# Performance work log

Hardware: AMD Instinct MI355X
Metric: run time of the kernel (lower is better)

The kernel has to match this reference:

```python
import jax, jax.numpy as jnp
import numpy as np

N = 1_000_000
C = 32
DIMS = (480, 360, 32)  # cylindrical voxel grid (z/rho, phi, height)
EPS = 1e-5


def setup_inputs() -> dict:
    rng = np.random.default_rng(0)
    total = DIMS[0] * DIMS[1] * DIMS[2]
    # unique active voxels, sorted so searchsorted gives row indices directly
    ids = np.sort(rng.choice(total, size=N, replace=False)).astype(np.int64)
    z = ids // (DIMS[1] * DIMS[2])
    rem = ids % (DIMS[1] * DIMS[2])
    y = rem // DIMS[2]
    x = rem % DIMS[2]
    coords = np.stack([z, y, x], axis=1)
    strides = np.array([DIMS[1] * DIMS[2], DIMS[2], 1], dtype=np.int64)

    def nbr(delta):
        out = np.full((3, N), -1, dtype=np.int32)
        for a in range(3):
            tgt = ids + delta * strides[a]
            ok = (coords[:, a] + delta >= 0) & (coords[:, a] + delta < DIMS[a])
            pos = np.searchsorted(ids, tgt)
            pos_c = np.clip(pos, 0, N - 1)
            found = ok & (ids[pos_c] == tgt)
            out[a] = np.where(found, pos_c, -1).astype(np.int32)
        return out

    nbr_prev = nbr(-1)
    nbr_next = nbr(+1)

    key = jax.random.key(0)
    k0, k1, k2 = jax.random.split(key, 3)
    features = jax.random.normal(k0, (N, C), dtype=jnp.float32)
    # W[branch, tap, in, out]; taps ordered (-1, 0, +1) along the branch's axis
    W = jax.random.normal(k1, (3, 3, C, C), dtype=jnp.float32) * (1.0 / np.sqrt(3 * C))
    gamma = jnp.ones((3, C), dtype=jnp.float32)
    beta = jnp.zeros((3, C), dtype=jnp.float32)
    mean = jax.random.normal(k2, (3, C), dtype=jnp.float32) * 0.1
    var = jnp.ones((3, C), dtype=jnp.float32)
    return {
        "features": features,
        "nbr_prev": jnp.asarray(nbr_prev),
        "nbr_next": jnp.asarray(nbr_next),
        "W": W,
        "gamma": gamma,
        "beta": beta,
        "mean": mean,
        "var": var,
    }


def _branch(f, Wb, prev, nxt, g, b, m, v):
    # 3-tap submanifold conv along one axis: gather prev/next active neighbors
    pm = prev >= 0
    nm = nxt >= 0
    fp = jnp.where(pm[:, None], f[jnp.where(pm, prev, 0)], 0.0)
    fn = jnp.where(nm[:, None], f[jnp.where(nm, nxt, 0)], 0.0)
    out = fp @ Wb[0] + f @ Wb[1] + fn @ Wb[2]
    # BatchNorm1d (inference stats) + Sigmoid
    out = (out - m) * (g * jax.lax.rsqrt(v + EPS)) + b
    return jax.nn.sigmoid(out)


def reference(features, nbr_prev, nbr_next, W, gamma, beta, mean, var):
    acc = jnp.zeros_like(features)
    for a in range(3):  # conv3x1x1, conv1x3x1, conv1x1x3
        acc = acc + _branch(features, W[a], nbr_prev[a], nbr_next[a],
                            gamma[a], beta[a], mean[a], var[a])
    return acc * features  # sparse_add then gating with input features
```

## Files before the change

kernel.cpp:

```cpp
#include <hip/hip_runtime.h>
#include <stdint.h>


typedef __attribute__((ext_vector_type(8))) __bf16 bf16x8;
typedef __attribute__((ext_vector_type(8))) unsigned short u16x8;
typedef __attribute__((ext_vector_type(4))) float f32x4;
typedef __attribute__((ext_vector_type(2))) float f32x2;

constexpr int NVOX    = 1000000;
constexpr int NTILES  = NVOX / 16;
constexpr int WPB     = 4;
constexpr float LOG2E = 1.4426950408889634f;

constexpr int TPW4     = 4;
constexpr int NWAVES4  = NTILES / TPW4;
constexpr int NBLOCKS4 = (NWAVES4 + WPB - 1) / WPB;

constexpr int TPW2     = 2;
constexpr int NWAVES2  = (NTILES + TPW2 - 1) / TPW2;
constexpr int NBLOCKS2 = (NWAVES2 + WPB - 1) / WPB;

constexpr int    WS_WELEMS = 18 * 64 * 8;
constexpr size_t FB_BYTES  = (size_t)NVOX * 64;
constexpr unsigned ZOFF    = (unsigned)(FB_BYTES + 18432 + 768);
constexpr size_t WS_NEED   = FB_BYTES + 18432 + 768 + 128;

__global__ __launch_bounds__(256) void prep_kernel(
    const float* __restrict__ Wt,
    const float* __restrict__ gma, const float* __restrict__ bta,
    const float* __restrict__ mea, const float* __restrict__ var,
    unsigned short* __restrict__ wsW, float* __restrict__ wsA,
    float* __restrict__ wsB, float* __restrict__ wsZ)
{
    int tid = blockIdx.x * 256 + threadIdx.x;
    if (tid < WS_WELEMS) {
        int f    = tid >> 9;
        int rem  = tid & 511;
        int lane = rem >> 3;
        int j    = rem & 7;
        int br = f / 6, t = (f >> 1) % 3, h = f & 1;
        int n = lane & 15, quad = lane >> 4;
        float w = Wt[((br * 3 + t) * 32 + quad * 8 + j) * 32 + 2 * n + h];
        union { float f; unsigned u; } c; c.f = w;
        wsW[(f * 64 + lane) * 8 + j] = (unsigned short)((c.u + 0x8000u) >> 16);
    } else if (tid < WS_WELEMS + 96) {
        int i = tid - WS_WELEMS;
        float s = gma[i] * __frsqrt_rn(var[i] + 1e-5f);
        wsA[i] = -s * LOG2E;
        wsB[i] = (mea[i] * s - bta[i]) * LOG2E;
    } else if (wsZ != nullptr && tid < WS_WELEMS + 96 + 32) {
        wsZ[tid - WS_WELEMS - 96] = 0.0f;
    }
}

__device__ __forceinline__ unsigned pack_bf(float a, float b) {
    union { float f; unsigned u; } ca, cb; ca.f = a; cb.f = b;
    return __builtin_amdgcn_perm(cb.u + 0x8000u, ca.u + 0x8000u, 0x07060302u);
}
__device__ __forceinline__ bf16x8 cvt_frag(f32x4 lo, f32x4 hi) {
    union { unsigned u[4]; bf16x8 v; } r;
    r.u[0] = pack_bf(lo[0], lo[1]); r.u[1] = pack_bf(lo[2], lo[3]);
    r.u[2] = pack_bf(hi[0], hi[1]); r.u[3] = pack_bf(hi[2], hi[3]);
    return r.v;
}

__global__ __launch_bounds__(256) void cvt_feat(
    const float* __restrict__ f, unsigned short* __restrict__ fb)
{
    int tid = blockIdx.x * 256 + threadIdx.x;
    const f32x4* p = (const f32x4*)(f + (size_t)tid * 8);
    f32x4 lo = p[0], hi = p[1];
    union { unsigned u[4]; u16x8 v; } r;
    r.u[0] = pack_bf(lo[0], lo[1]); r.u[1] = pack_bf(lo[2], lo[3]);
    r.u[2] = pack_bf(hi[0], hi[1]); r.u[3] = pack_bf(hi[2], hi[3]);
    *(u16x8*)(fb + (size_t)tid * 8) = r.v;
}

__device__ __forceinline__ f32x4 mfma16(u16x8 a, bf16x8 b, f32x4 c) {
    return __builtin_amdgcn_mfma_f32_16x16x32_bf16(
        __builtin_bit_cast(bf16x8, a), b, c, 0, 0, 0);
}

__global__ __launch_bounds__(256) void recon_bf16(
    const float* __restrict__ feat,
    const int*   __restrict__ nprev,
    const int*   __restrict__ nnext,
    const char*  __restrict__ fbc,
    const unsigned short* __restrict__ wsW,
    const float* __restrict__ wsA,
    const float* __restrict__ wsB,
    float*       __restrict__ out)
{
    __shared__ unsigned short smem[WS_WELEMS];
    {
        const u16x8* s = (const u16x8*)wsW;
        u16x8* d = (u16x8*)smem;
        #pragma unroll
        for (int i = 0; i < 5; ++i) {
            int k = (int)threadIdx.x + i * 256;
            if (k < 18 * 64) d[k] = s[k];
        }
    }
    __syncthreads();

    const int lane = threadIdx.x & 63;
    const int n    = lane & 15;
    const int quad = lane >> 4;
    const unsigned qo = (unsigned)quad * 16u;

    int b   = blockIdx.x;
    int per = NBLOCKS4 / 8;
    int bs  = (b < per * 8) ? ((b & 7) * per + (b >> 3)) : b;
    int wv  = bs * WPB + (threadIdx.x >> 6);
    if (wv >= NWAVES4) return;
    const int t0 = wv * TPW4;

    f32x2 A_[3], B_[3];
    #pragma unroll
    for (int br = 0; br < 3; ++br) {
        A_[br] = *(const f32x2*)(wsA + br * 32 + 2 * n);
        B_[br] = *(const f32x2*)(wsB + br * 32 + 2 * n);
    }

    unsigned lbase = (unsigned)lane * 16u;

    int idxP[2][3], idxN[2][3];
    {
        int r0 = t0 * 16 + n;
        #pragma unroll
        for (int a = 0; a < 3; ++a) {
            idxP[0][a] = nprev[a * NVOX + r0];
            idxN[0][a] = nnext[a * NVOX + r0];
            idxP[1][a] = nprev[a * NVOX + r0 + 16];
            idxN[1][a] = nnext[a * NVOX + r0 + 16];
        }
    }

    u16x8 G[2][7];
    {
        int row0 = t0 * 16 + n;
        G[0][0] = *(const u16x8*)(fbc + (unsigned)row0 * 64u + qo);
        #pragma unroll
        for (int a = 0; a < 3; ++a) {
            unsigned op = idxP[0][a] >= 0 ? (unsigned)idxP[0][a] * 64u : ZOFF;
            unsigned on = idxN[0][a] >= 0 ? (unsigned)idxN[0][a] * 64u : ZOFF;
            G[0][1 + a] = *(const u16x8*)(fbc + op + qo);
            G[0][4 + a] = *(const u16x8*)(fbc + on + qo);
        }
    }

    #pragma unroll
    for (int tt = 0; tt < TPW4; ++tt) {
        const int cur  = tt & 1;
        const int nxt  = cur ^ 1;
        const int base = (t0 + tt) * 16;

        f32x2 fv[4];
        #pragma unroll
        for (int r = 0; r < 4; ++r)
            fv[r] = __builtin_nontemporal_load(
                (const f32x2*)(feat + (base + quad * 4 + r) * 32 + 2 * n));

        if (tt + 1 < TPW4) {
            int rown = base + 16 + n;
            G[nxt][0] = *(const u16x8*)(fbc + (unsigned)rown * 64u + qo);
            #pragma unroll
            for (int a = 0; a < 3; ++a) {
                unsigned op = idxP[nxt][a] >= 0 ? (unsigned)idxP[nxt][a] * 64u : ZOFF;
                unsigned on = idxN[nxt][a] >= 0 ? (unsigned)idxN[nxt][a] * 64u : ZOFF;
                G[nxt][1 + a] = *(const u16x8*)(fbc + op + qo);
                G[nxt][4 + a] = *(const u16x8*)(fbc + on + qo);
            }
        }
        if (tt + 2 < TPW4) {
            int r2 = base + 32 + n;
            #pragma unroll
            for (int a = 0; a < 3; ++a) {
                idxP[cur][a] = nprev[a * NVOX + r2];
                idxN[cur][a] = nnext[a * NVOX + r2];
            }
        }

        asm volatile("" : "+v"(lbase));
        const char* sb = (const char*)smem + lbase;

        f32x4 acc0 = {0.f, 0.f, 0.f, 0.f}, acc1 = {0.f, 0.f, 0.f, 0.f};
        #pragma unroll
        for (int br = 0; br < 3; ++br) {
            bf16x8 w0 = *(const bf16x8*)(sb + (br * 6 + 0) * 1024);
            bf16x8 w1 = *(const bf16x8*)(sb + (br * 6 + 1) * 1024);
            bf16x8 w2 = *(const bf16x8*)(sb + (br * 6 + 2) * 1024);
            bf16x8 w3 = *(const bf16x8*)(sb + (br * 6 + 3) * 1024);
            bf16x8 w4 = *(const bf16x8*)(sb + (br * 6 + 4) * 1024);
            bf16x8 w5 = *(const bf16x8*)(sb + (br * 6 + 5) * 1024);
            f32x4 c0 = {0.f, 0.f, 0.f, 0.f}, c1 = {0.f, 0.f, 0.f, 0.f};
            c0 = mfma16(G[cur][1 + br], w0, c0);
            c1 = mfma16(G[cur][1 + br], w1, c1);
            c0 = mfma16(G[cur][0],      w2, c0);
            c1 = mfma16(G[cur][0],      w3, c1);
            c0 = mfma16(G[cur][4 + br], w4, c0);
            c1 = mfma16(G[cur][4 + br], w5, c1);
            float a0 = A_[br][0], b0 = B_[br][0];
            float a1 = A_[br][1], b1 = B_[br][1];
            #pragma unroll
            for (int r = 0; r < 4; ++r) {
                float e0 = __builtin_amdgcn_exp2f(__builtin_fmaf(c0[r], a0, b0));
                float e1 = __builtin_amdgcn_exp2f(__builtin_fmaf(c1[r], a1, b1));
                acc0[r] += __builtin_amdgcn_rcpf(1.0f + e0);
                acc1[r] += __builtin_amdgcn_rcpf(1.0f + e1);
            }
        }

        #pragma unroll
        for (int r = 0; r < 4; ++r) {
            int vrow = base + quad * 4 + r;
            f32x2 ov = { acc0[r] * fv[r][0], acc1[r] * fv[r][1] };
            __builtin_nontemporal_store(ov, (f32x2*)(out + vrow * 32 + 2 * n));
        }
    }
}

__global__ __launch_bounds__(256) void recon_legacy(
    const float*          __restrict__ feat,
    const int*            __restrict__ nprev,
    const int*            __restrict__ nnext,
    const unsigned short* __restrict__ wsW,
    const float*          __restrict__ wsA,
    const float*          __restrict__ wsB,
    float*                __restrict__ out)
{
    const int lane = threadIdx.x & 63;
    const int n    = lane & 15;
    const int quad = lane >> 4;

    int b   = blockIdx.x;
    int per = NBLOCKS2 / 8;
    int bs  = (b < per * 8) ? ((b & 7) * per + (b >> 3)) : b;
    int wv  = bs * WPB + (threadIdx.x >> 6);

    const int t0 = wv * TPW2;
    if (t0 >= NTILES) return;

    bf16x8 Bf[18];
    #pragma unroll
    for (int f = 0; f < 18; ++f)
        Bf[f] = __builtin_bit_cast(bf16x8, *(const u16x8*)(wsW + (f * 64 + lane) * 8));

    f32x2 A_[3], B_[3];
    #pragma unroll
    for (int br = 0; br < 3; ++br) {
        A_[br] = *(const f32x2*)(wsA + br * 32 + 2 * n);
        B_[br] = *(const f32x2*)(wsB + br * 32 + 2 * n);
    }

    int ip[3], inx[3];
    {
        int row0 = t0 * 16 + n;
        #pragma unroll
        for (int a = 0; a < 3; ++a) {
            ip[a]  = nprev[a * NVOX + row0];
            inx[a] = nnext[a * NVOX + row0];
        }
    }

    #pragma unroll 1
    for (int tt = 0; tt < TPW2; ++tt) {
        int tile = t0 + tt;
        if (tile >= NTILES) break;
        int base = tile * 16;
        int row  = base + n;

        const f32x4* ps = (const f32x4*)(feat + row * 32 + quad * 8);
        f32x4 s_lo = ps[0], s_hi = ps[1];
        f32x4 p_lo[3], p_hi[3], n_lo[3], n_hi[3];
        #pragma unroll
        for (int a = 0; a < 3; ++a) {
            p_lo[a] = (f32x4){0.f, 0.f, 0.f, 0.f}; p_hi[a] = p_lo[a];
            n_lo[a] = p_lo[a];                     n_hi[a] = p_lo[a];
            if (ip[a] >= 0) {
                const f32x4* pp = (const f32x4*)(feat + ip[a] * 32 + quad * 8);
                p_lo[a] = pp[0]; p_hi[a] = pp[1];
            }
            if (inx[a] >= 0) {
                const f32x4* pn = (const f32x4*)(feat + inx[a] * 32 + quad * 8);
                n_lo[a] = pn[0]; n_hi[a] = pn[1];
            }
        }

        int ipn[3], inn[3];
        if (tt + 1 < TPW2 && tile + 1 < NTILES) {
            int nrow = row + 16;
            #pragma unroll
            for (int a = 0; a < 3; ++a) {
                ipn[a] = nprev[a * NVOX + nrow];
                inn[a] = nnext[a * NVOX + nrow];
            }
        } else {
            #pragma unroll
            for (int a = 0; a < 3; ++a) { ipn[a] = -1; inn[a] = -1; }
        }

        bf16x8 Aself = cvt_frag(s_lo, s_hi);
        bf16x8 Ap[3], An[3];
        #pragma unroll
        for (int a = 0; a < 3; ++a) {
            Ap[a] = cvt_frag(p_lo[a], p_hi[a]);
            An[a] = cvt_frag(n_lo[a], n_hi[a]);
        }

        f32x4 acc0 = {0.f, 0.f, 0.f, 0.f}, acc1 = {0.f, 0.f, 0.f, 0.f};
        #pragma unroll
        for (int br = 0; br < 3; ++br) {
            f32x4 c0 = {0.f, 0.f, 0.f, 0.f}, c1 = {0.f, 0.f, 0.f, 0.f};
            c0 = __builtin_amdgcn_mfma_f32_16x16x32_bf16(Ap[br], Bf[br*6 + 0], c0, 0, 0, 0);
            c1 = __builtin_amdgcn_mfma_f32_16x16x32_bf16(Ap[br], Bf[br*6 + 1], c1, 0, 0, 0);
            c0 = __builtin_amdgcn_mfma_f32_16x16x32_bf16(Aself,  Bf[br*6 + 2], c0, 0, 0, 0);
            c1 = __builtin_amdgcn_mfma_f32_16x16x32_bf16(Aself,  Bf[br*6 + 3], c1, 0, 0, 0);
            c0 = __builtin_amdgcn_mfma_f32_16x16x32_bf16(An[br], Bf[br*6 + 4], c0, 0, 0, 0);
            c1 = __builtin_amdgcn_mfma_f32_16x16x32_bf16(An[br], Bf[br*6 + 5], c1, 0, 0, 0);
            float a0 = A_[br][0], b0 = B_[br][0], a1 = A_[br][1], b1 = B_[br][1];
            #pragma unroll
            for (int r = 0; r < 4; ++r) {
                float e0 = __builtin_amdgcn_exp2f(__builtin_fmaf(c0[r], a0, b0));
                float e1 = __builtin_amdgcn_exp2f(__builtin_fmaf(c1[r], a1, b1));
                acc0[r] += __builtin_amdgcn_rcpf(1.0f + e0);
                acc1[r] += __builtin_amdgcn_rcpf(1.0f + e1);
            }
        }

        #pragma unroll
        for (int r = 0; r < 4; ++r) {
            int vrow = base + quad * 4 + r;
            f32x2 fv = *(const f32x2*)(feat + vrow * 32 + 2 * n);
            f32x2 ov = { acc0[r] * fv[0], acc1[r] * fv[1] };
            *(f32x2*)(out + vrow * 32 + 2 * n) = ov;
        }

        #pragma unroll
        for (int a = 0; a < 3; ++a) { ip[a] = ipn[a]; inx[a] = inn[a]; }
    }
}

extern "C" void kernel_launch(void* const* d_in, const int* in_sizes, int n_in,
                              void* d_out, int out_size, void* d_ws, size_t ws_size,
                              hipStream_t stream) {
    const float* feat  = (const float*)d_in[0];
    const int*   nprev = (const int*)d_in[1];
    const int*   nnext = (const int*)d_in[2];
    const float* Wt    = (const float*)d_in[3];
    const float* gma   = (const float*)d_in[4];
    const float* bta   = (const float*)d_in[5];
    const float* mea   = (const float*)d_in[6];
    const float* var   = (const float*)d_in[7];
    float*       o     = (float*)d_out;

    if (ws_size >= WS_NEED) {
        unsigned short* fb  = (unsigned short*)d_ws;
        unsigned short* wsW = (unsigned short*)((char*)d_ws + FB_BYTES);
        float* wsA = (float*)((char*)d_ws + FB_BYTES + 18432);
        float* wsB = wsA + 96;
        float* wsZ = wsB + 96;
        prep_kernel<<<(WS_WELEMS + 96 + 32 + 255) / 256, 256, 0, stream>>>(
            Wt, gma, bta, mea, var, wsW, wsA, wsB, wsZ);
        cvt_feat<<<(NVOX * 32) / (256 * 8), 256, 0, stream>>>(feat, fb);
        recon_bf16<<<NBLOCKS4, 256, 0, stream>>>(feat, nprev, nnext,
            (const char*)d_ws, wsW, wsA, wsB, o);
    } else {
        unsigned short* wsW = (unsigned short*)d_ws;
        float* wsA = (float*)((char*)d_ws + WS_WELEMS * 2);
        float* wsB = wsA + 96;
        prep_kernel<<<(WS_WELEMS + 96 + 255) / 256, 256, 0, stream>>>(
            Wt, gma, bta, mea, var, wsW, wsA, wsB, nullptr);
        recon_legacy<<<NBLOCKS2, 256, 0, stream>>>(feat, nprev, nnext,
                                                   wsW, wsA, wsB, o);
    }
}
```

Before: 304.8 us.

## Fuse weight prep with feature bf16 conversion and raise tiles per wave

Result: no change. 305.9 us (+0.4%).

```diff
diff --git a/kernel.cpp b/kernel.cpp
--- a/kernel.cpp
+++ b/kernel.cpp
@@ -12,9 +12,9 @@
 constexpr int WPB     = 4;
 constexpr float LOG2E = 1.4426950408889634f;
 
-constexpr int TPW4     = 4;
-constexpr int NWAVES4  = NTILES / TPW4;
-constexpr int NBLOCKS4 = (NWAVES4 + WPB - 1) / WPB;
+constexpr int TPWF     = 5;
+constexpr int NWAVESF  = NTILES / TPWF;
+constexpr int NBLOCKSF = NWAVESF / WPB;
 
 constexpr int TPW2     = 2;
 constexpr int NWAVES2  = (NTILES + TPW2 - 1) / TPW2;
@@ -25,7 +25,44 @@
 constexpr unsigned ZOFF    = (unsigned)(FB_BYTES + 18432 + 768);
 constexpr size_t WS_NEED   = FB_BYTES + 18432 + 768 + 128;
 
-__global__ __launch_bounds__(256) void prep_kernel(
+constexpr int CVT_THREADS = NVOX * 32 / 16;
+constexpr int PREP_TAIL   = WS_WELEMS + 96 + 32;
+constexpr int PREPALL_BLK = (CVT_THREADS + PREP_TAIL + 255) / 256;
+
+__device__ __forceinline__ unsigned pack_bf(float a, float b) {
+    union { float f; unsigned u; } ca, cb; ca.f = a; cb.f = b;
+    return __builtin_amdgcn_perm(cb.u + 0x8000u, ca.u + 0x8000u, 0x07060302u);
+}
+
+__device__ __forceinline__ void prep_tail_work(
+    int t, const float* __restrict__ Wt,
+    const float* __restrict__ gma, const float* __restrict__ bta,
+    const float* __restrict__ mea, const float* __restrict__ var,
+    unsigned short* __restrict__ wsW, float* __restrict__ wsA,
+    float* __restrict__ wsB, float* __restrict__ wsZ)
+{
+    if (t < WS_WELEMS) {
+        int f    = t >> 9;
+        int rem  = t & 511;
+        int lane = rem >> 3;
+        int j    = rem & 7;
+        int br = f / 6, tap = (f >> 1) % 3, h = f & 1;
+        int n = lane & 15, quad = lane >> 4;
+        float w = Wt[((br * 3 + tap) * 32 + quad * 8 + j) * 32 + 2 * n + h];
+        union { float f; unsigned u; } c; c.f = w;
+        wsW[(f * 64 + lane) * 8 + j] = (unsigned short)((c.u + 0x8000u) >> 16);
+    } else if (t < WS_WELEMS + 96) {
+        int i = t - WS_WELEMS;
+        float s = gma[i] * __frsqrt_rn(var[i] + 1e-5f);
+        wsA[i] = -s * LOG2E;
+        wsB[i] = (mea[i] * s - bta[i]) * LOG2E;
+    } else if (wsZ != nullptr && t < WS_WELEMS + 96 + 32) {
+        wsZ[t - WS_WELEMS - 96] = 0.0f;
+    }
+}
+
+__global__ __launch_bounds__(256) void prep_all(
+    const float* __restrict__ feat, unsigned short* __restrict__ fb,
     const float* __restrict__ Wt,
     const float* __restrict__ gma, const float* __restrict__ bta,
     const float* __restrict__ mea, const float* __restrict__ var,
@@ -33,47 +70,38 @@
     float* __restrict__ wsB, float* __restrict__ wsZ)
 {
     int tid = blockIdx.x * 256 + threadIdx.x;
-    if (tid < WS_WELEMS) {
-        int f    = tid >> 9;
-        int rem  = tid & 511;
-        int lane = rem >> 3;
-        int j    = rem & 7;
-        int br = f / 6, t = (f >> 1) % 3, h = f & 1;
-        int n = lane & 15, quad = lane >> 4;
-        float w = Wt[((br * 3 + t) * 32 + quad * 8 + j) * 32 + 2 * n + h];
-        union { float f; unsigned u; } c; c.f = w;
-        wsW[(f * 64 + lane) * 8 + j] = (unsigned short)((c.u + 0x8000u) >> 16);
-    } else if (tid < WS_WELEMS + 96) {
-        int i = tid - WS_WELEMS;
-        float s = gma[i] * __frsqrt_rn(var[i] + 1e-5f);
-        wsA[i] = -s * LOG2E;
-        wsB[i] = (mea[i] * s - bta[i]) * LOG2E;
-    } else if (wsZ != nullptr && tid < WS_WELEMS + 96 + 32) {
-        wsZ[tid - WS_WELEMS - 96] = 0.0f;
-    }
-}
-
-__device__ __forceinline__ unsigned pack_bf(float a, float b) {
-    union { float f; unsigned u; } ca, cb; ca.f = a; cb.f = b;
-    return __builtin_amdgcn_perm(cb.u + 0x8000u, ca.u + 0x8000u, 0x07060302u);
-}
+    if (tid < CVT_THREADS) {
+        const f32x4* p = (const f32x4*)(feat + (size_t)tid * 16);
+        f32x4 v0 = p[0], v1 = p[1], v2 = p[2], v3 = p[3];
+        union { unsigned u[8]; u16x8 v[2]; } r;
+        r.u[0] = pack_bf(v0[0], v0[1]); r.u[1] = pack_bf(v0[2], v0[3]);
+        r.u[2] = pack_bf(v1[0], v1[1]); r.u[3] = pack_bf(v1[2], v1[3]);
+        r.u[4] = pack_bf(v2[0], v2[1]); r.u[5] = pack_bf(v2[2], v2[3]);
+        r.u[6] = pack_bf(v3[0], v3[1]); r.u[7] = pack_bf(v3[2], v3[3]);
+        u16x8* q = (u16x8*)(fb + (size_t)tid * 16);
+        q[0] = r.v[0]; q[1] = r.v[1];
+    } else {
+        prep_tail_work(tid - CVT_THREADS, Wt, gma, bta, mea, var,
+                       wsW, wsA, wsB, wsZ);
+    }
+}
+
+__global__ __launch_bounds__(256) void prep_kernel(
+    const float* __restrict__ Wt,
+    const float* __restrict__ gma, const float* __restrict__ bta,
+    const float* __restrict__ mea, const float* __restrict__ var,
+    unsigned short* __restrict__ wsW, float* __restrict__ wsA,
+    float* __restrict__ wsB)
+{
+    int tid = blockIdx.x * 256 + threadIdx.x;
+    prep_tail_work(tid, Wt, gma, bta, mea, var, wsW, wsA, wsB, nullptr);
+}
+
 __device__ __forceinline__ bf16x8 cvt_frag(f32x4 lo, f32x4 hi) {
     union { unsigned u[4]; bf16x8 v; } r;
     r.u[0] = pack_bf(lo[0], lo[1]); r.u[1] = pack_bf(lo[2], lo[3]);
     r.u[2] = pack_bf(hi[0], hi[1]); r.u[3] = pack_bf(hi[2], hi[3]);
     return r.v;
-}
-
-__global__ __launch_bounds__(256) void cvt_feat(
-    const float* __restrict__ f, unsigned short* __restrict__ fb)
-{
-    int tid = blockIdx.x * 256 + threadIdx.x;
-    const f32x4* p = (const f32x4*)(f + (size_t)tid * 8);
-    f32x4 lo = p[0], hi = p[1];
-    union { unsigned u[4]; u16x8 v; } r;
-    r.u[0] = pack_bf(lo[0], lo[1]); r.u[1] = pack_bf(lo[2], lo[3]);
-    r.u[2] = pack_bf(hi[0], hi[1]); r.u[3] = pack_bf(hi[2], hi[3]);
-    *(u16x8*)(fb + (size_t)tid * 8) = r.v;
 }
 
 __device__ __forceinline__ f32x4 mfma16(u16x8 a, bf16x8 b, f32x4 c) {
@@ -109,11 +137,11 @@
     const unsigned qo = (unsigned)quad * 16u;
 
     int b   = blockIdx.x;
-    int per = NBLOCKS4 / 8;
+    int per = NBLOCKSF / 8;
     int bs  = (b < per * 8) ? ((b & 7) * per + (b >> 3)) : b;
     int wv  = bs * WPB + (threadIdx.x >> 6);
-    if (wv >= NWAVES4) return;
-    const int t0 = wv * TPW4;
+    if (wv >= NWAVESF) return;
+    const int t0 = wv * TPWF;
 
     f32x2 A_[3], B_[3];
     #pragma unroll
@@ -129,10 +157,10 @@
         int r0 = t0 * 16 + n;
         #pragma unroll
         for (int a = 0; a < 3; ++a) {
-            idxP[0][a] = nprev[a * NVOX + r0];
-            idxN[0][a] = nnext[a * NVOX + r0];
-            idxP[1][a] = nprev[a * NVOX + r0 + 16];
-            idxN[1][a] = nnext[a * NVOX + r0 + 16];
+            idxP[0][a] = __builtin_nontemporal_load(nprev + a * NVOX + r0);
+            idxN[0][a] = __builtin_nontemporal_load(nnext + a * NVOX + r0);
+            idxP[1][a] = __builtin_nontemporal_load(nprev + a * NVOX + r0 + 16);
+            idxN[1][a] = __builtin_nontemporal_load(nnext + a * NVOX + r0 + 16);
         }
     }
 
@@ -150,7 +178,7 @@
     }
 
     #pragma unroll
-    for (int tt = 0; tt < TPW4; ++tt) {
+    for (int tt = 0; tt < TPWF; ++tt) {
         const int cur  = tt & 1;
         const int nxt  = cur ^ 1;
         const int base = (t0 + tt) * 16;
@@ -161,7 +189,7 @@
             fv[r] = __builtin_nontemporal_load(
                 (const f32x2*)(feat + (base + quad * 4 + r) * 32 + 2 * n));
 
-        if (tt + 1 < TPW4) {
+        if (tt + 1 < TPWF) {
             int rown = base + 16 + n;
             G[nxt][0] = *(const u16x8*)(fbc + (unsigned)rown * 64u + qo);
             #pragma unroll
@@ -172,12 +200,12 @@
                 G[nxt][4 + a] = *(const u16x8*)(fbc + on + qo);
             }
         }
-        if (tt + 2 < TPW4) {
+        if (tt + 2 < TPWF) {
             int r2 = base + 32 + n;
             #pragma unroll
             for (int a = 0; a < 3; ++a) {
-                idxP[cur][a] = nprev[a * NVOX + r2];
-                idxN[cur][a] = nnext[a * NVOX + r2];
+                idxP[cur][a] = __builtin_nontemporal_load(nprev + a * NVOX + r2);
+                idxN[cur][a] = __builtin_nontemporal_load(nnext + a * NVOX + r2);
             }
         }
 
@@ -360,17 +388,16 @@
         float* wsA = (float*)((char*)d_ws + FB_BYTES + 18432);
         float* wsB = wsA + 96;
         float* wsZ = wsB + 96;
-        prep_kernel<<<(WS_WELEMS + 96 + 32 + 255) / 256, 256, 0, stream>>>(
-            Wt, gma, bta, mea, var, wsW, wsA, wsB, wsZ);
-        cvt_feat<<<(NVOX * 32) / (256 * 8), 256, 0, stream>>>(feat, fb);
-        recon_bf16<<<NBLOCKS4, 256, 0, stream>>>(feat, nprev, nnext,
+        prep_all<<<PREPALL_BLK, 256, 0, stream>>>(
+            feat, fb, Wt, gma, bta, mea, var, wsW, wsA, wsB, wsZ);
+        recon_bf16<<<NBLOCKSF, 256, 0, stream>>>(feat, nprev, nnext,
             (const char*)d_ws, wsW, wsA, wsB, o);
     } else {
         unsigned short* wsW = (unsigned short*)d_ws;
         float* wsA = (float*)((char*)d_ws + WS_WELEMS * 2);
         float* wsB = wsA + 96;
-        prep_kernel<<<(WS_WELEMS + 96 + 255) / 256, 256, 0, stream>>>(
-            Wt, gma, bta, mea, var, wsW, wsA, wsB, nullptr);
+        prep_kernel<<<(PREP_TAIL + 255) / 256, 256, 0, stream>>>(
+            Wt, gma, bta, mea, var, wsW, wsA, wsB);
         recon_legacy<<<NBLOCKS2, 256, 0, stream>>>(feat, nprev, nnext,
                                                    wsW, wsA, wsB, o);
     }
```
